# Kernel tuning notes

Measured on AMD Instinct MI355X. Metric: run time of the kernel, lower is better.

Reference implementation:

```python
import jax, jax.numpy as jnp
import numpy as np

WEIGHT = 2e-9       # lambda for the CRF loss
SIGMA_RGB = 15.0    # appearance (color) bandwidth
SIGMA_XY = 100.0    # spatial bandwidth (scaled by SCALE inside the loss, as in the torch module)
SCALE = 0.5         # scale_factor for both image and segmentation


def _nearest_resize(x, sf):
    # torch F.interpolate(mode='nearest'): src_idx = floor(dst_idx / sf)
    H, W = x.shape[-2:]
    Ho, Wo = int(H * sf), int(W * sf)
    iy = jnp.floor(jnp.arange(Ho) / sf).astype(jnp.int32)
    ix = jnp.floor(jnp.arange(Wo) / sf).astype(jnp.int32)
    return x[:, :, iy][:, :, :, ix]


def _bilinear_resize(x, sf):
    # torch F.interpolate(mode='bilinear', align_corners=False): src = (dst+0.5)/sf - 0.5
    N, C, H, W = x.shape
    Ho, Wo = int(H * sf), int(W * sf)

    def axis_idx(n_in, n_out):
        s = (jnp.arange(n_out, dtype=x.dtype) + 0.5) * (n_in / n_out) - 0.5
        s = jnp.clip(s, 0.0, n_in - 1)
        i0 = jnp.floor(s).astype(jnp.int32)
        i1 = jnp.minimum(i0 + 1, n_in - 1)
        w = (s - i0).astype(x.dtype)
        return i0, i1, w

    y0, y1, wy = axis_idx(H, Ho)
    x0, x1, wx = axis_idx(W, Wo)
    xr = x[:, :, y0, :] * (1.0 - wy)[None, None, :, None] + x[:, :, y1, :] * wy[None, None, :, None]
    return xr[:, :, :, x0] * (1.0 - wx) + xr[:, :, :, x1] * wx


def _dense_crf_loss(images, segmentations):
    img = _nearest_resize(images, SCALE)          # [N,3,H,W], values in [0,255]
    seg = _bilinear_resize(segmentations, SCALE)  # [N,K,H,W]
    N, Kc, H, W = seg.shape
    P = H * W
    sxy = SIGMA_XY * SCALE

    yy, xx = jnp.meshgrid(jnp.arange(H, dtype=img.dtype), jnp.arange(W, dtype=img.dtype), indexing='ij')
    pos = jnp.stack([xx, yy], 0) / sxy                       # [2,H,W]
    pos = jnp.broadcast_to(pos[None], (N, 2, H, W))
    feats = jnp.concatenate([pos, img / SIGMA_RGB], axis=1)  # [N,5,H,W]
    feats = feats.reshape(N, 5, P).transpose(0, 2, 1)        # [N,P,5]

    # dense bilateral (Gaussian) kernel: K[p,q] = exp(-||f_p - f_q||^2 / 2)
    sq = jnp.sum(feats * feats, axis=-1)                     # [N,P]
    d2 = sq[:, :, None] + sq[:, None, :] - 2.0 * jnp.einsum('npd,nqd->npq', feats, feats)
    Kmat = jnp.exp(-0.5 * jnp.maximum(d2, 0.0))              # [N,P,P]

    S = seg.reshape(N, Kc, P)                                # [N,K,P]
    AS = jnp.einsum('npq,nkq->nkp', Kmat, S)                 # filtered segmentations
    loss = -jnp.sum(S * AS) / N
    return jnp.reshape(WEIGHT * loss, (1,))


def setup_inputs() -> dict:
    key = jax.random.key(0)
    k1, k2 = jax.random.split(key)
    images = jax.random.uniform(k1, (4, 3, 128, 128), jnp.float32) * 255.0
    logits = jax.random.normal(k2, (4, 2, 128, 128), jnp.float32)
    segmentations = jax.nn.softmax(logits, axis=1)  # softmaxed logits, as per docstring
    return {"images": images, "segmentations": segmentations}


def reference(images, segmentations):
    return _dense_crf_loss(images, segmentations)
```

## Files before the change

kernel.cpp:

```cpp
#include <hip/hip_runtime.h>


#define NIMG 4
#define HW   64
#define PP   (HW * HW)
#define HIN  128
#define PT   256
#define QT   512
#define NPT  (PP / PT)
#define NQT  (PP / QT)

__global__ __launch_bounds__(256)
void crf_pre(const float* __restrict__ img, const float* __restrict__ seg,
             float4* __restrict__ pts, float* __restrict__ out) {
    int idx = blockIdx.x * 256 + threadIdx.x;
    if (idx == 0) out[0] = 0.0f;
    if (idx >= NIMG * PP) return;
    int n = idx / PP, p = idx % PP;
    int y = p >> 6, x = p & 63;

    const float inv_sxy = 1.0f / 50.0f;
    const float inv_rgb = 1.0f / 15.0f;
    float fx = (float)x * inv_sxy;
    float fy = (float)y * inv_sxy;

    int iy = 2 * y, ix = 2 * x;
    const float* ib = img + (size_t)n * 3 * HIN * HIN;
    float r = ib[(0 * HIN + iy) * HIN + ix] * inv_rgb;
    float g = ib[(1 * HIN + iy) * HIN + ix] * inv_rgb;
    float b = ib[(2 * HIN + iy) * HIN + ix] * inv_rgb;

    const float* sb = seg + (size_t)n * 2 * HIN * HIN;
    float s0, s1;
    {
        const float2* r0 = (const float2*)(sb + (0 * HIN + iy) * HIN + ix);
        const float2* r1 = (const float2*)(sb + (0 * HIN + iy + 1) * HIN + ix);
        float2 a0 = r0[0], a1 = r1[0];
        s0 = 0.25f * ((a0.x + a0.y) + (a1.x + a1.y));
    }
    {
        const float2* r0 = (const float2*)(sb + (1 * HIN + iy) * HIN + ix);
        const float2* r1 = (const float2*)(sb + (1 * HIN + iy + 1) * HIN + ix);
        float2 a0 = r0[0], a1 = r1[0];
        s1 = 0.25f * ((a0.x + a0.y) + (a1.x + a1.y));
    }

    float c0 = -0.5f * (fx * fx + fy * fy + r * r + g * g + b * b);

    float4 v0 = make_float4(fx, fy, r, g);
    float4 v1 = make_float4(b, c0, s0, s1);
    pts[(size_t)idx * 2 + 0] = v0;
    pts[(size_t)idx * 2 + 1] = v1;
}

__global__ __launch_bounds__(256)
void crf_main(const float4* __restrict__ pts, float* __restrict__ out) {
    __shared__ float4 qs[QT * 2];
    __shared__ float wsum[4];

    int bid = blockIdx.x;
    int qi = bid % NQT;
    int t  = bid / NQT;
    int pi = t % NPT;
    int n  = t / NPT;

    const float4* src = pts + (size_t)(n * PP + qi * QT) * 2;
    for (int j = threadIdx.x; j < QT * 2; j += 256) qs[j] = src[j];

    int p = pi * PT + threadIdx.x;
    const float4 a = pts[(size_t)(n * PP + p) * 2 + 0];
    const float4 b = pts[(size_t)(n * PP + p) * 2 + 1];
    __syncthreads();

    float acc = 0.0f;
#pragma unroll 4
    for (int q = 0; q < QT; ++q) {
        float4 qa = qs[2 * q + 0];
        float4 qb = qs[2 * q + 1];
        float arg = b.y + qb.y;
        arg = fmaf(a.x, qa.x, arg);
        arg = fmaf(a.y, qa.y, arg);
        arg = fmaf(a.z, qa.z, arg);
        arg = fmaf(a.w, qa.w, arg);
        arg = fmaf(b.x, qb.x, arg);
        float k  = __expf(arg);
        float sd = fmaf(b.z, qb.z, b.w * qb.w);
        acc = fmaf(k, sd, acc);
    }

    for (int off = 32; off; off >>= 1) acc += __shfl_down(acc, off, 64);
    if ((threadIdx.x & 63) == 0) wsum[threadIdx.x >> 6] = acc;
    __syncthreads();
    if (threadIdx.x == 0) {
        float s = ((wsum[0] + wsum[1]) + (wsum[2] + wsum[3]));
        atomicAdd(out, s * (-2e-9f / (float)NIMG));
    }
}

extern "C" void kernel_launch(void* const* d_in, const int* in_sizes, int n_in,
                              void* d_out, int out_size, void* d_ws, size_t ws_size,
                              hipStream_t stream) {
    const float* img = (const float*)d_in[0];
    const float* seg = (const float*)d_in[1];
    float* out = (float*)d_out;
    float4* pts = (float4*)d_ws;

    crf_pre<<<(NIMG * PP) / 256, 256, 0, stream>>>(img, seg, pts, out);
    crf_main<<<NIMG * NPT * NQT, 256, 0, stream>>>(pts, out);
}
```

Before: 84.05 us.

## Register-block four p points per thread and use exp2 with folded log2e

Each thread now handles four p points held in registers, so every q element read from shared memory is reused four times, and the q tile shrinks to 128 points. The exponent is moved to base 2 by folding log2(e) into the p features and the precomputed constant, which lets the raw exp2 builtin replace __expf. The segmentation dot product is split into two per-class accumulators that are combined once after the loop, removing a multiply from the inner loop. In exchange, register pressure per thread rises and the grid has fewer blocks, each doing more work.

```diff
diff --git a/kernel.cpp b/kernel.cpp
--- a/kernel.cpp
+++ b/kernel.cpp
@@ -5,10 +5,12 @@
 #define HW   64
 #define PP   (HW * HW)
 #define HIN  128
-#define PT   256
-#define QT   512
-#define NPT  (PP / PT)
-#define NQT  (PP / QT)
+#define MB   4
+#define PTILE (256 * MB)
+#define QTILE 128
+#define NPT  (PP / PTILE)
+#define NQT  (PP / QTILE)
+#define LOG2E 1.44269504088896f
 
 __global__ __launch_bounds__(256)
 void crf_pre(const float* __restrict__ img, const float* __restrict__ seg,
@@ -45,7 +47,7 @@
         s1 = 0.25f * ((a0.x + a0.y) + (a1.x + a1.y));
     }
 
-    float c0 = -0.5f * (fx * fx + fy * fy + r * r + g * g + b * b);
+    float c0 = -0.5f * LOG2E * (fx * fx + fy * fy + r * r + g * g + b * b);
 
     float4 v0 = make_float4(fx, fy, r, g);
     float4 v1 = make_float4(b, c0, s0, s1);
@@ -55,7 +57,7 @@
 
 __global__ __launch_bounds__(256)
 void crf_main(const float4* __restrict__ pts, float* __restrict__ out) {
-    __shared__ float4 qs[QT * 2];
+    __shared__ float4 qs[QTILE * 2];
     __shared__ float wsum[4];
 
     int bid = blockIdx.x;
@@ -64,29 +66,48 @@
     int pi = t % NPT;
     int n  = t / NPT;
 
-    const float4* src = pts + (size_t)(n * PP + qi * QT) * 2;
-    for (int j = threadIdx.x; j < QT * 2; j += 256) qs[j] = src[j];
+    const float4* src = pts + (size_t)(n * PP + qi * QTILE) * 2;
+    qs[threadIdx.x] = src[threadIdx.x];
 
-    int p = pi * PT + threadIdx.x;
-    const float4 a = pts[(size_t)(n * PP + p) * 2 + 0];
-    const float4 b = pts[(size_t)(n * PP + p) * 2 + 1];
+    float pax[MB], pay[MB], paz[MB], paw[MB], pbx[MB];
+    float pc0[MB], ps0[MB], ps1[MB];
+    float acc0[MB], acc1[MB];
+#pragma unroll
+    for (int m = 0; m < MB; ++m) {
+        int p = pi * PTILE + m * 256 + threadIdx.x;
+        float4 a = pts[(size_t)(n * PP + p) * 2 + 0];
+        float4 b = pts[(size_t)(n * PP + p) * 2 + 1];
+        pax[m] = a.x * LOG2E; pay[m] = a.y * LOG2E;
+        paz[m] = a.z * LOG2E; paw[m] = a.w * LOG2E;
+        pbx[m] = b.x * LOG2E;
+        pc0[m] = b.y;
+        ps0[m] = b.z; ps1[m] = b.w;
+        acc0[m] = 0.0f; acc1[m] = 0.0f;
+    }
     __syncthreads();
 
-    float acc = 0.0f;
-#pragma unroll 4
-    for (int q = 0; q < QT; ++q) {
+#pragma unroll 2
+    for (int q = 0; q < QTILE; ++q) {
         float4 qa = qs[2 * q + 0];
         float4 qb = qs[2 * q + 1];
-        float arg = b.y + qb.y;
-        arg = fmaf(a.x, qa.x, arg);
-        arg = fmaf(a.y, qa.y, arg);
-        arg = fmaf(a.z, qa.z, arg);
-        arg = fmaf(a.w, qa.w, arg);
-        arg = fmaf(b.x, qb.x, arg);
-        float k  = __expf(arg);
-        float sd = fmaf(b.z, qb.z, b.w * qb.w);
-        acc = fmaf(k, sd, acc);
+#pragma unroll
+        for (int m = 0; m < MB; ++m) {
+            float arg = pc0[m] + qb.y;
+            arg = fmaf(pax[m], qa.x, arg);
+            arg = fmaf(pay[m], qa.y, arg);
+            arg = fmaf(paz[m], qa.z, arg);
+            arg = fmaf(paw[m], qa.w, arg);
+            arg = fmaf(pbx[m], qb.x, arg);
+            float k = __builtin_amdgcn_exp2f(arg);
+            acc0[m] = fmaf(k, qb.z, acc0[m]);
+            acc1[m] = fmaf(k, qb.w, acc1[m]);
+        }
     }
+
+    float acc = 0.0f;
+#pragma unroll
+    for (int m = 0; m < MB; ++m)
+        acc += fmaf(ps0[m], acc0[m], ps1[m] * acc1[m]);
 
     for (int off = 32; off; off >>= 1) acc += __shfl_down(acc, off, 64);
     if ((threadIdx.x & 63) == 0) wsum[threadIdx.x >> 6] = acc;
```

Result: faster. 78.40 us (-6.7%).
